# Optimization experiments

Hardware: AMD Instinct MI355X
Metric: run time of the kernel (lower is better)

Reference implementation:

```python
import jax, jax.numpy as jnp
import numpy as np

N, E, D, H = 50000, 500000, 128, 128


def setup_inputs() -> dict:
    key = jax.random.key(0)
    ks = jax.random.split(key, 20)
    s = 0.05
    inp = {
        "node_states": jax.random.normal(ks[0], (N, D), jnp.float32),
        "edge_features": jax.random.normal(ks[1], (E, D), jnp.float32),
        "from_idx": jax.random.randint(ks[2], (E,), 0, N, dtype=jnp.int32),
        "to_idx": jax.random.randint(ks[3], (E,), 0, N, dtype=jnp.int32),
        "graph_idx": jax.random.randint(ks[4], (N,), 0, 16, dtype=jnp.int32),
        # message MLP: Linear(3D,H)-ReLU-Linear(H,H)-ReLU-Linear(H,D)
        "mW1": jax.random.normal(ks[5], (3 * D, H), jnp.float32) * s,
        "mb1": jnp.zeros((H,), jnp.float32),
        "mW2": jax.random.normal(ks[6], (H, H), jnp.float32) * s,
        "mb2": jnp.zeros((H,), jnp.float32),
        "mW3": jax.random.normal(ks[7], (H, D), jnp.float32) * s,
        "mb3": jnp.zeros((D,), jnp.float32),
    }
    # three GRU cells; W: input->gates [D,3D], U: hidden->gates [D,3D]; gate order r,z,n (torch)
    for i, g in enumerate(["g0", "g1", "g2"]):
        inp[g + "W"] = jax.random.normal(ks[8 + 2 * i], (D, 3 * D), jnp.float32) * s
        inp[g + "U"] = jax.random.normal(ks[9 + 2 * i], (D, 3 * D), jnp.float32) * s
        inp[g + "b"] = jnp.zeros((3 * D,), jnp.float32)
        inp[g + "c"] = jnp.zeros((3 * D,), jnp.float32)
    return inp


def _mlp(x, W1, b1, W2, b2, W3, b3):
    h = jax.nn.relu(x @ W1 + b1)
    h = jax.nn.relu(h @ W2 + b2)
    return h @ W3 + b3


def _gru(x, h, W, U, b, c):
    gi = x @ W + b  # [N,3D]
    gh = h @ U + c
    ir, iz, inn = jnp.split(gi, 3, axis=1)
    hr, hz, hn = jnp.split(gh, 3, axis=1)
    r = jax.nn.sigmoid(ir + hr)
    z = jax.nn.sigmoid(iz + hz)
    n = jnp.tanh(inn + r * hn)
    return (1.0 - z) * n + z * h


def reference(node_states, edge_features, from_idx, to_idx, graph_idx,
              mW1, mb1, mW2, mb2, mW3, mb3,
              g0W, g0U, g0b, g0c, g1W, g1U, g1b, g1c, g2W, g2U, g2b, g2c):
    n_nodes = node_states.shape[0]

    def prop_once(fi, ti):
        edge_in = jnp.concatenate(
            [node_states[fi], node_states[ti], edge_features], axis=1)  # [E,3D]
        edge_states = _mlp(edge_in, mW1, mb1, mW2, mb2, mW3, mb3)  # [E,D]
        return jax.ops.segment_sum(edge_states, ti, num_segments=n_nodes)

    # forward uses self.message_net for BOTH directions (reverse net unused)
    agg = prop_once(from_idx, to_idx) + prop_once(to_idx, from_idx)  # [N,D]

    h1 = _gru(node_states, agg, g0W, g0U, g0b, g0c)
    h2 = _gru(agg, h1, g1W, g1U, g1b, g1c)
    h3 = _gru(h1, h2, g2W, g2U, g2b, g2c)
    return h3
```

## Files before the change

kernel.cpp:

```cpp
#include <hip/hip_runtime.h>

typedef unsigned short u16;
typedef __attribute__((ext_vector_type(8))) short bf16x8;
typedef __attribute__((ext_vector_type(4))) float f32x4;

__device__ inline u16 f2bf(float f) {
  unsigned int u = __float_as_uint(f);
  u += 0x7fffu + ((u >> 16) & 1u);
  return (u16)(u >> 16);
}
__device__ inline float bf2f(u16 v) {
  return __uint_as_float((unsigned)v << 16);
}

__device__ inline uint4 pack8(float4 a, float4 b) {
  uint4 r;
  r.x = (unsigned)f2bf(a.x) | ((unsigned)f2bf(a.y) << 16);
  r.y = (unsigned)f2bf(a.z) | ((unsigned)f2bf(a.w) << 16);
  r.z = (unsigned)f2bf(b.x) | ((unsigned)f2bf(b.y) << 16);
  r.w = (unsigned)f2bf(b.z) | ((unsigned)f2bf(b.w) << 16);
  return r;
}

struct TransDesc {
  const float* src[9];
  u16* dst[9];
  int R[9];
  int C[9];
  int pre[10];
};

__global__ void transpose_all_kernel(TransDesc td) {
  int t = blockIdx.x * 256 + threadIdx.x;
  if (t >= td.pre[9]) return;
  int seg = 0;
  while (t >= td.pre[seg + 1]) ++seg;
  int local = t - td.pre[seg];
  int C = td.C[seg], R = td.R[seg];
  int r = local / C, c = local - r * C;
  td.dst[seg][(size_t)c * R + r] = f2bf(td.src[seg][local]);
}

__global__ void count_kernel(const int* __restrict__ fi,
                             const int* __restrict__ ti,
                             int* __restrict__ cnt, int E) {
  int e = blockIdx.x * 256 + threadIdx.x;
  if (e < E) {
    atomicAdd(&cnt[ti[e]], 1);
    atomicAdd(&cnt[fi[e]], 1);
  }
}

__global__ void scan1_kernel(const int* __restrict__ cnt,
                             int* __restrict__ partial, int N, int chunk) {
  __shared__ int sdata[256];
  int b = blockIdx.x, t = threadIdx.x;
  int base = b * chunk;
  int sum = 0;
  for (int i = t; i < chunk; i += 256) {
    int idx = base + i;
    if (idx < N) sum += cnt[idx];
  }
  sdata[t] = sum;
  __syncthreads();
  for (int s2 = 128; s2 > 0; s2 >>= 1) {
    if (t < s2) sdata[t] += sdata[t + s2];
    __syncthreads();
  }
  if (t == 0) partial[b] = sdata[0];
}

__global__ void scan2_kernel(int* __restrict__ partial) {
  __shared__ int s[256];
  int t = threadIdx.x;
  int own = partial[t];
  s[t] = own;
  __syncthreads();
  for (int d2 = 1; d2 < 256; d2 <<= 1) {
    int v = (t >= d2) ? s[t - d2] : 0;
    __syncthreads();
    s[t] += v;
    __syncthreads();
  }
  partial[t] = s[t] - own;
}

__global__ void scan3_kernel(const int* __restrict__ cnt,
                             const int* __restrict__ partialEx,
                             int* __restrict__ cursor, int N, int chunk) {
  __shared__ int s[256];
  int b = blockIdx.x, t = threadIdx.x;
  int base = b * chunk;
  int own = (t < chunk && base + t < N) ? cnt[base + t] : 0;
  s[t] = own;
  __syncthreads();
  for (int d2 = 1; d2 < 256; d2 <<= 1) {
    int v = (t >= d2) ? s[t - d2] : 0;
    __syncthreads();
    s[t] += v;
    __syncthreads();
  }
  int ex = s[t] - own + partialEx[b];
  if (t < chunk && base + t < N) cursor[base + t] = ex;
}

__global__ void slot_kernel(const int* __restrict__ fi,
                            const int* __restrict__ ti,
                            int* __restrict__ cursor, int* __restrict__ s_nbr,
                            int* __restrict__ s_eid, int* __restrict__ s_dest,
                            int E) {
  int e = blockIdx.x * 256 + threadIdx.x;
  if (e < E) {
    int f = fi[e], t2 = ti[e];
    int p0 = atomicAdd(&cursor[t2], 1);
    s_nbr[p0] = f;
    s_eid[p0] = e;
    s_dest[p0] = t2;
    int p1 = atomicAdd(&cursor[f], 1);
    s_nbr[p1] = t2;
    s_eid[p1] = e;
    s_dest[p1] = f;
  }
}

__device__ inline void stage_w_rw(u16* sW, const u16* __restrict__ src,
                                  int roww, int colofs, int tid) {
  int n = tid >> 1, half = tid & 1;
  const u16* s = src + (size_t)n * roww + colofs + half * 64;
#pragma unroll
  for (int q = 0; q < 8; ++q) {
    uint4 v = *(const uint4*)(s + q * 8);
    int byte = n * 256 + ((half * 128 + q * 16) ^ ((n & 7) << 4));
    *(uint4*)((char*)sW + byte) = v;
  }
}

__device__ inline void stage_w_512(u16* sW, const u16* __restrict__ src,
                                   int roww, int colofs, int tid) {
  int n = tid >> 2, quarter = tid & 3;
  const u16* s = src + (size_t)n * roww + colofs + quarter * 32;
#pragma unroll
  for (int q = 0; q < 4; ++q) {
    uint4 v = *(const uint4*)(s + q * 8);
    int byte = n * 256 + ((quarter * 64 + q * 16) ^ ((n & 7) << 4));
    *(uint4*)((char*)sW + byte) = v;
  }
}

__device__ inline void mfma_pass(const u16* A, const u16* W, f32x4 acc[8],
                                 int w, int lane) {
  const int cA = lane & 15;
  const int ko = (lane >> 4) * 8;
  const int arow = 16 * w + cA;
#pragma unroll
  for (int kk = 0; kk < 4; ++kk) {
    int ka = (kk * 32 + ko) * 2;
    int sx = ka ^ ((cA & 7) << 4);
    bf16x8 a = *(const bf16x8*)((const char*)A + arow * 256 + sx);
#pragma unroll
    for (int nt = 0; nt < 8; ++nt) {
      bf16x8 bb = *(const bf16x8*)((const char*)W + (nt * 16 + cA) * 256 + sx);
      acc[nt] = __builtin_amdgcn_mfma_f32_16x16x32_bf16(a, bb, acc[nt], 0, 0, 0);
    }
  }
}

__device__ inline void write_h_lds(u16* sH, const f32x4 acc[8], int w,
                                   int lane) {
#pragma unroll
  for (int nt = 0; nt < 8; ++nt) {
    int col = nt * 16 + (lane & 15);
#pragma unroll
    for (int i = 0; i < 4; ++i) {
      int rr = 16 * w + ((lane >> 4) * 4) + i;
      *(u16*)((char*)sH + rr * 256 + ((col * 2) ^ ((rr & 7) << 4))) =
          f2bf(acc[nt][i]);
    }
  }
}

__global__ __launch_bounds__(256) void gemm1_kernel(
    const float* __restrict__ ns, const float* __restrict__ ef,
    const u16* __restrict__ Wt1, const float* __restrict__ b1,
    u16* __restrict__ Pa, u16* __restrict__ Pb, u16* __restrict__ EFm, int N,
    int E, int Nb) {
  __shared__ u16 sA[64 * 128];
  __shared__ u16 sW[128 * 128];
  const int tid = threadIdx.x;
  const int lane = tid & 63;
  const int w = tid >> 6;
  if ((int)blockIdx.x < Nb) {
    const int r0 = blockIdx.x * 64;
    {
      int row = tid >> 2, seg = tid & 3;
      int rr = r0 + row;
      if (rr >= N) rr = N - 1;
      const float4* sx = (const float4*)(ns + (size_t)rr * 128 + seg * 32);
#pragma unroll
      for (int q = 0; q < 4; ++q) {
        int byte = row * 256 + ((seg * 64 + q * 16) ^ ((row & 7) << 4));
        *(uint4*)((char*)sA + byte) = pack8(sx[q * 2], sx[q * 2 + 1]);
      }
    }
    stage_w_rw(sW, Wt1, 384, 0, tid);
    __syncthreads();
    f32x4 accA[8] = {};
    mfma_pass(sA, sW, accA, w, lane);
    __syncthreads();
    stage_w_rw(sW, Wt1, 384, 128, tid);
    __syncthreads();
    f32x4 accB[8] = {};
    mfma_pass(sA, sW, accB, w, lane);
#pragma unroll
    for (int nt = 0; nt < 8; ++nt) {
      int col = nt * 16 + (lane & 15);
#pragma unroll
      for (int i = 0; i < 4; ++i) {
        int rr = 16 * w + ((lane >> 4) * 4) + i;
        int row = r0 + rr;
        if (row < N) {
          Pa[(size_t)row * 128 + col] = f2bf(accA[nt][i]);
          Pb[(size_t)row * 128 + col] = f2bf(accB[nt][i]);
        }
      }
    }
  } else {
    const int r0 = (blockIdx.x - Nb) * 64;
    {
      int row = tid >> 2, seg = tid & 3;
      int rr = r0 + row;
      if (rr >= E) rr = E - 1;
      const float4* sx = (const float4*)(ef + (size_t)rr * 128 + seg * 32);
#pragma unroll
      for (int q = 0; q < 4; ++q) {
        int byte = row * 256 + ((seg * 64 + q * 16) ^ ((row & 7) << 4));
        *(uint4*)((char*)sA + byte) = pack8(sx[q * 2], sx[q * 2 + 1]);
      }
    }
    stage_w_rw(sW, Wt1, 384, 256, tid);
    __syncthreads();
    f32x4 acc[8] = {};
    mfma_pass(sA, sW, acc, w, lane);
    __syncthreads();
#pragma unroll
    for (int nt = 0; nt < 8; ++nt) {
      int col = nt * 16 + (lane & 15);
      float bv = b1[col];
#pragma unroll
      for (int i = 0; i < 4; ++i) {
        int rr = 16 * w + ((lane >> 4) * 4) + i;
        *(u16*)((char*)sA + rr * 256 + ((col * 2) ^ ((rr & 7) << 4))) =
            f2bf(acc[nt][i] + bv);
      }
    }
    __syncthreads();
#pragma unroll
    for (int it = 0; it < 4; ++it) {
      int task = tid + (it << 8);
      int row = task >> 4, c8 = task & 15;
      int gr = r0 + row;
      if (gr < E) {
        uint4 v = *(const uint4*)((const char*)sA + row * 256 +
                                  ((c8 << 4) ^ ((row & 7) << 4)));
        *(uint4*)(EFm + (size_t)gr * 128 + (c8 << 3)) = v;
      }
    }
  }
}

__global__ __launch_bounds__(512, 2) void edge_csr2_kernel(
    const u16* __restrict__ EFm, const int* __restrict__ s_nbr,
    const int* __restrict__ s_eid, const int* __restrict__ s_dest,
    const u16* __restrict__ Wt2, const u16* __restrict__ Wt3,
    const u16* __restrict__ Pa, const u16* __restrict__ Pb,
    const float* __restrict__ b2, const float* __restrict__ b3,
    float* __restrict__ aggf, int nslots, int ntiles) {
  __shared__ u16 sW2[128 * 128];
  __shared__ u16 sW3[128 * 128];
  __shared__ u16 sH[64 * 128];
  const int tid = threadIdx.x;
  const int lane = tid & 63;
  const int wv = tid >> 6;
  const int mw = wv >> 1;
  const int nw = wv & 1;
  const int l15 = lane & 15;
  const int lhi = lane >> 4;

  stage_w_512(sW2, Wt2, 128, 0, tid);
  stage_w_512(sW3, Wt3, 128, 0, tid);
  float b2f[4], b3f[4];
#pragma unroll
  for (int nt = 0; nt < 4; ++nt) {
    int col = (nw << 6) + (nt << 4) + l15;
    b2f[nt] = b2[col];
    b3f[nt] = b3[col];
  }
  __syncthreads();

  const int ra = (mw << 4) + l15;

  for (int t = blockIdx.x; t < ntiles; t += gridDim.x) {
    const int r0 = t << 6;
#pragma unroll
    for (int it = 0; it < 2; ++it) {
      int task = tid + (it << 9);
      int row = task >> 4;
      int c8 = task & 15;
      int r = r0 + row;
      int rc = r < nslots ? r : nslots - 1;
      int nbr = s_nbr[rc], eid = s_eid[rc], dst = s_dest[rc];
      uint4 efv = *(const uint4*)(EFm + (size_t)eid * 128 + (c8 << 3));
      uint4 pav = *(const uint4*)(Pa + (size_t)nbr * 128 + (c8 << 3));
      uint4 pbv = *(const uint4*)(Pb + (size_t)dst * 128 + (c8 << 3));
      const u16* pe = (const u16*)&efv;
      const u16* pa = (const u16*)&pav;
      const u16* pb = (const u16*)&pbv;
      unsigned o[4];
#pragma unroll
      for (int j = 0; j < 4; ++j) {
        float v0 = fmaxf(bf2f(pe[2 * j]) + bf2f(pa[2 * j]) + bf2f(pb[2 * j]), 0.f);
        float v1 = fmaxf(bf2f(pe[2 * j + 1]) + bf2f(pa[2 * j + 1]) + bf2f(pb[2 * j + 1]), 0.f);
        o[j] = (unsigned)f2bf(v0) | ((unsigned)f2bf(v1) << 16);
      }
      *(uint4*)((char*)sH + row * 256 + ((c8 << 4) ^ ((row & 7) << 4))) = *(uint4*)o;
    }
    __syncthreads();
    bf16x8 hA[4];
#pragma unroll
    for (int kk = 0; kk < 4; ++kk) {
      int sx = ((kk << 6) + (lhi << 4)) ^ ((ra & 7) << 4);
      hA[kk] = *(const bf16x8*)((const char*)sH + ra * 256 + sx);
    }
    f32x4 acc[4] = {};
#pragma unroll
    for (int kk = 0; kk < 4; ++kk) {
#pragma unroll
      for (int nt = 0; nt < 4; ++nt) {
        int c = (nw << 6) + (nt << 4) + l15;
        int sx = ((kk << 6) + (lhi << 4)) ^ ((c & 7) << 4);
        bf16x8 bb = *(const bf16x8*)((const char*)sW2 + c * 256 + sx);
        acc[nt] = __builtin_amdgcn_mfma_f32_16x16x32_bf16(hA[kk], bb, acc[nt], 0, 0, 0);
      }
    }
    __syncthreads();
#pragma unroll
    for (int i = 0; i < 4; ++i) {
      int rl = (mw << 4) + (lhi << 2) + i;
#pragma unroll
      for (int nt = 0; nt < 4; ++nt) {
        int col = (nw << 6) + (nt << 4) + l15;
        float v = fmaxf(acc[nt][i] + b2f[nt], 0.f);
        *(u16*)((char*)sH + rl * 256 + ((col * 2) ^ ((rl & 7) << 4))) = f2bf(v);
        acc[nt][i] = 0.f;
      }
    }
    __syncthreads();
#pragma unroll
    for (int kk = 0; kk < 4; ++kk) {
      int sx = ((kk << 6) + (lhi << 4)) ^ ((ra & 7) << 4);
      hA[kk] = *(const bf16x8*)((const char*)sH + ra * 256 + sx);
    }
#pragma unroll
    for (int kk = 0; kk < 4; ++kk) {
#pragma unroll
      for (int nt = 0; nt < 4; ++nt) {
        int c = (nw << 6) + (nt << 4) + l15;
        int sx = ((kk << 6) + (lhi << 4)) ^ ((c & 7) << 4);
        bf16x8 bb = *(const bf16x8*)((const char*)sW3 + c * 256 + sx);
        acc[nt] = __builtin_amdgcn_mfma_f32_16x16x32_bf16(hA[kk], bb, acc[nt], 0, 0, 0);
      }
    }
    __syncthreads();
#pragma unroll
    for (int i = 0; i < 4; ++i) {
      int rl = (mw << 4) + (lhi << 2) + i;
#pragma unroll
      for (int nt = 0; nt < 4; ++nt) {
        int col = (nw << 6) + (nt << 4) + l15;
        *(u16*)((char*)sH + rl * 256 + ((col * 2) ^ ((rl & 7) << 4))) =
            f2bf(acc[nt][i] + b3f[nt]);
      }
    }
    __syncthreads();
    {
      int c = tid & 127, q = tid >> 7;
      float s = 0.f;
      int prev = -1;
      int rbeg = q << 4;
#pragma unroll 4
      for (int rr = rbeg; rr < rbeg + 16; ++rr) {
        int r = r0 + rr;
        int d = (r < nslots) ? s_dest[r] : -1;
        if (d != prev) {
          if (prev >= 0) unsafeAtomicAdd(&aggf[(size_t)prev * 128 + c], s);
          prev = d;
          s = 0.f;
        }
        if (d >= 0)
          s += bf2f(*(const u16*)((const char*)sH + rr * 256 +
                                  ((c * 2) ^ ((rr & 7) << 4))));
      }
      if (prev >= 0) unsafeAtomicAdd(&aggf[(size_t)prev * 128 + c], s);
    }
    __syncthreads();
  }
}

__global__ __launch_bounds__(512, 1) void gru3_kernel(
    const float* __restrict__ ns, const float* __restrict__ aggf,
    const u16* __restrict__ g0W, const u16* __restrict__ g0U,
    const u16* __restrict__ g1W, const u16* __restrict__ g1U,
    const u16* __restrict__ g2W, const u16* __restrict__ g2U,
    const float* __restrict__ b0, const float* __restrict__ c0,
    const float* __restrict__ b1, const float* __restrict__ c1,
    const float* __restrict__ b2, const float* __restrict__ c2,
    float* __restrict__ out, int N) {
  __shared__ u16 sX[128 * 128];
  __shared__ u16 sG[128 * 128];
  __shared__ u16 sW[128 * 128];
  const int tid = threadIdx.x;
  const int lane = tid & 63;
  const int w = tid >> 6;
  const int r0 = blockIdx.x * 128;
  {
    int row = tid >> 2, seg = tid & 3;
    int rr = r0 + row;
    if (rr >= N) rr = N - 1;
    const float4* sx = (const float4*)(ns + (size_t)rr * 128 + seg * 32);
    const float4* sh = (const float4*)(aggf + (size_t)rr * 128 + seg * 32);
#pragma unroll
    for (int q = 0; q < 4; ++q) {
      int byte = row * 256 + ((seg * 64 + q * 16) ^ ((row & 7) << 4));
      *(uint4*)((char*)sX + byte) = pack8(sx[q * 2], sx[q * 2 + 1]);
      *(uint4*)((char*)sG + byte) = pack8(sh[q * 2], sh[q * 2 + 1]);
    }
  }

  float hpf[8][4];

#define GPASS(SRC, ABUF, ACC)                       \
  __syncthreads();                                  \
  stage_w_512(sW, (SRC), 128, 0, tid);              \
  __syncthreads();                                  \
  mfma_pass((ABUF), sW, (ACC), w, lane);

  {
    f32x4 ar[8] = {}, az[8] = {}, ai[8] = {}, ah[8] = {};
    GPASS(g0W + 0 * 16384, sX, ar)
    GPASS(g0U + 0 * 16384, sG, ar)
    GPASS(g0W + 1 * 16384, sX, az)
    GPASS(g0U + 1 * 16384, sG, az)
    GPASS(g0W + 2 * 16384, sX, ai)
    GPASS(g0U + 2 * 16384, sG, ah)
    f32x4 h1[8];
#pragma unroll
    for (int nt = 0; nt < 8; ++nt) {
      int col = nt * 16 + (lane & 15);
      float brc = b0[col] + c0[col];
      float bzc = b0[128 + col] + c0[128 + col];
      float bi = b0[256 + col];
      float bc2 = c0[256 + col];
#pragma unroll
      for (int i = 0; i < 4; ++i) {
        int rloc = 16 * w + ((lane >> 4) * 4) + i;
        int row = r0 + rloc;
        int rowc = row < N ? row : N - 1;
        float hf = aggf[(size_t)rowc * 128 + col];
        float rg = 1.f / (1.f + __expf(-(ar[nt][i] + brc)));
        float zg = 1.f / (1.f + __expf(-(az[nt][i] + bzc)));
        float pre = ai[nt][i] + bi + rg * (ah[nt][i] + bc2);
        float ng = 2.f / (1.f + __expf(-2.f * pre)) - 1.f;
        float hv = (1.f - zg) * ng + zg * hf;
        h1[nt][i] = hv;
        hpf[nt][i] = hv;
      }
    }
    write_h_lds(sX, h1, w, lane);
  }
  {
    f32x4 ar[8] = {}, az[8] = {}, ai[8] = {}, ah[8] = {};
    GPASS(g1W + 0 * 16384, sG, ar)
    GPASS(g1U + 0 * 16384, sX, ar)
    GPASS(g1W + 1 * 16384, sG, az)
    GPASS(g1U + 1 * 16384, sX, az)
    GPASS(g1W + 2 * 16384, sG, ai)
    GPASS(g1U + 2 * 16384, sX, ah)
    f32x4 h2[8];
#pragma unroll
    for (int nt = 0; nt < 8; ++nt) {
      int col = nt * 16 + (lane & 15);
      float brc = b1[col] + c1[col];
      float bzc = b1[128 + col] + c1[128 + col];
      float bi = b1[256 + col];
      float bc2 = c1[256 + col];
#pragma unroll
      for (int i = 0; i < 4; ++i) {
        float rg = 1.f / (1.f + __expf(-(ar[nt][i] + brc)));
        float zg = 1.f / (1.f + __expf(-(az[nt][i] + bzc)));
        float pre = ai[nt][i] + bi + rg * (ah[nt][i] + bc2);
        float ng = 2.f / (1.f + __expf(-2.f * pre)) - 1.f;
        float hv = (1.f - zg) * ng + zg * hpf[nt][i];
        h2[nt][i] = hv;
        hpf[nt][i] = hv;
      }
    }
    write_h_lds(sG, h2, w, lane);
  }
  {
    f32x4 ar[8] = {}, az[8] = {}, ai[8] = {}, ah[8] = {};
    GPASS(g2W + 0 * 16384, sX, ar)
    GPASS(g2U + 0 * 16384, sG, ar)
    GPASS(g2W + 1 * 16384, sX, az)
    GPASS(g2U + 1 * 16384, sG, az)
    GPASS(g2W + 2 * 16384, sX, ai)
    GPASS(g2U + 2 * 16384, sG, ah)
#pragma unroll
    for (int nt = 0; nt < 8; ++nt) {
      int col = nt * 16 + (lane & 15);
      float brc = b2[col] + c2[col];
      float bzc = b2[128 + col] + c2[128 + col];
      float bi = b2[256 + col];
      float bc2 = c2[256 + col];
#pragma unroll
      for (int i = 0; i < 4; ++i) {
        int rloc = 16 * w + ((lane >> 4) * 4) + i;
        int row = r0 + rloc;
        if (row < N) {
          float rg = 1.f / (1.f + __expf(-(ar[nt][i] + brc)));
          float zg = 1.f / (1.f + __expf(-(az[nt][i] + bzc)));
          float pre = ai[nt][i] + bi + rg * (ah[nt][i] + bc2);
          float ng = 2.f / (1.f + __expf(-2.f * pre)) - 1.f;
          out[(size_t)row * 128 + col] = (1.f - zg) * ng + zg * hpf[nt][i];
        }
      }
    }
  }
#undef GPASS
}

extern "C" void kernel_launch(void* const* d_in, const int* in_sizes, int n_in,
                              void* d_out, int out_size, void* d_ws,
                              size_t ws_size, hipStream_t stream) {
  const float* ns = (const float*)d_in[0];
  const float* ef = (const float*)d_in[1];
  const int* from_idx = (const int*)d_in[2];
  const int* to_idx = (const int*)d_in[3];
  const float* mW1 = (const float*)d_in[5];
  const float* mb1 = (const float*)d_in[6];
  const float* mW2 = (const float*)d_in[7];
  const float* mb2 = (const float*)d_in[8];
  const float* mW3 = (const float*)d_in[9];
  const float* mb3 = (const float*)d_in[10];
  const float* gW[3] = {(const float*)d_in[11], (const float*)d_in[15], (const float*)d_in[19]};
  const float* gU[3] = {(const float*)d_in[12], (const float*)d_in[16], (const float*)d_in[20]};
  const float* gb[3] = {(const float*)d_in[13], (const float*)d_in[17], (const float*)d_in[21]};
  const float* gc[3] = {(const float*)d_in[14], (const float*)d_in[18], (const float*)d_in[22]};

  const int N = in_sizes[0] / 128;
  const int E = in_sizes[1] / 128;
  const int nslots = 2 * E;

  char* base = (char*)d_ws;
  size_t cur = 0;
  auto alloc = [&](size_t bytes) {
    size_t p = cur;
    cur = (cur + bytes + 255) & ~(size_t)255;
    return (void*)(base + p);
  };
  float* aggf = (float*)alloc((size_t)N * 128 * 4);
  u16* Pa = (u16*)alloc((size_t)N * 128 * 2);
  u16* Pb = (u16*)alloc((size_t)N * 128 * 2);
  u16* Wt1 = (u16*)alloc(384 * 128 * 2);
  u16* Wt2 = (u16*)alloc(128 * 128 * 2);
  u16* Wt3 = (u16*)alloc(128 * 128 * 2);
  u16 *gWt[3], *gUt[3];
  for (int i = 0; i < 3; ++i) {
    gWt[i] = (u16*)alloc(384 * 128 * 2);
    gUt[i] = (u16*)alloc(384 * 128 * 2);
  }
  int* cnt = (int*)alloc((size_t)N * 4);
  int* cursor = (int*)alloc((size_t)N * 4);
  int* partial = (int*)alloc(256 * 4);
  int* s_nbr = (int*)alloc((size_t)nslots * 4);
  int* s_eid = (int*)alloc((size_t)nslots * 4);
  int* s_dest = (int*)alloc((size_t)nslots * 4);
  u16* EFm = (u16*)alloc((size_t)E * 128 * 2);
  (void)ws_size;

  {
    TransDesc td;
    const float* srcs[9] = {mW1, mW2, mW3, gW[0], gU[0], gW[1], gU[1], gW[2], gU[2]};
    u16* dsts[9] = {Wt1, Wt2, Wt3, gWt[0], gUt[0], gWt[1], gUt[1], gWt[2], gUt[2]};
    int Rs[9] = {384, 128, 128, 128, 128, 128, 128, 128, 128};
    int Cs[9] = {128, 128, 128, 384, 384, 384, 384, 384, 384};
    int acc = 0;
    for (int i = 0; i < 9; ++i) {
      td.src[i] = srcs[i];
      td.dst[i] = dsts[i];
      td.R[i] = Rs[i];
      td.C[i] = Cs[i];
      td.pre[i] = acc;
      acc += Rs[i] * Cs[i];
    }
    td.pre[9] = acc;
    transpose_all_kernel<<<(acc + 255) / 256, 256, 0, stream>>>(td);
  }

  hipMemsetAsync(cnt, 0, (size_t)N * 4, stream);
  count_kernel<<<(E + 255) / 256, 256, 0, stream>>>(from_idx, to_idx, cnt, E);
  int chunk = (N + 255) / 256;
  scan1_kernel<<<256, 256, 0, stream>>>(cnt, partial, N, chunk);
  scan2_kernel<<<1, 256, 0, stream>>>(partial);
  scan3_kernel<<<256, 256, 0, stream>>>(cnt, partial, cursor, N, chunk);
  slot_kernel<<<(E + 255) / 256, 256, 0, stream>>>(from_idx, to_idx, cursor,
                                                   s_nbr, s_eid, s_dest, E);

  int Nb = (N + 63) / 64, Eb = (E + 63) / 64;
  gemm1_kernel<<<Nb + Eb, 256, 0, stream>>>(ns, ef, Wt1, mb1, Pa, Pb, EFm, N,
                                            E, Nb);

  hipMemsetAsync(aggf, 0, (size_t)N * 128 * 4, stream);
  int ntiles = (nslots + 63) / 64;
  int egrid = ntiles < 512 ? ntiles : 512;
  edge_csr2_kernel<<<egrid, 512, 0, stream>>>(EFm, s_nbr, s_eid, s_dest, Wt2,
                                              Wt3, Pa, Pb, mb2, mb3, aggf,
                                              nslots, ntiles);

  int gblocks = (N + 127) / 128;
  gru3_kernel<<<gblocks, 512, 0, stream>>>(
      ns, aggf, gWt[0], gUt[0], gWt[1], gUt[1], gWt[2], gUt[2], gb[0], gc[0],
      gb[1], gc[1], gb[2], gc[2], (float*)d_out, N);
}
```

Measured before the change: 632.3 us.

## Read GRU weights directly from global and enlarge gemm1 tiles to 128 rows

The GRU kernel no longer stages each weight slice into LDS behind barriers. MFMA B-operands are now read straight from global/L2, with 64-row blocks of 256 threads and two blocks per CU. Gate computation is reordered (r and n first, then z) so fewer accumulator sets are live at once, lowering register pressure. gemm1 now uses 512-thread blocks over 128-row tiles, so each staged weight tile serves twice as many rows. The cost is uncoalesced global weight loads in the GRU, which depend on cache hits.

```diff
diff --git a/kernel.cpp b/kernel.cpp
--- a/kernel.cpp
+++ b/kernel.cpp
@@ -123,18 +123,6 @@
   }
 }
 
-__device__ inline void stage_w_rw(u16* sW, const u16* __restrict__ src,
-                                  int roww, int colofs, int tid) {
-  int n = tid >> 1, half = tid & 1;
-  const u16* s = src + (size_t)n * roww + colofs + half * 64;
-#pragma unroll
-  for (int q = 0; q < 8; ++q) {
-    uint4 v = *(const uint4*)(s + q * 8);
-    int byte = n * 256 + ((half * 128 + q * 16) ^ ((n & 7) << 4));
-    *(uint4*)((char*)sW + byte) = v;
-  }
-}
-
 __device__ inline void stage_w_512(u16* sW, const u16* __restrict__ src,
                                    int roww, int colofs, int tid) {
   int n = tid >> 2, quarter = tid & 3;
@@ -165,6 +153,25 @@
   }
 }
 
+__device__ inline void mfma_pass_g(const u16* A, const u16* __restrict__ Wg,
+                                   f32x4 acc[8], int w, int lane) {
+  const int cA = lane & 15;
+  const int ko = (lane >> 4) * 8;
+  const int arow = 16 * w + cA;
+#pragma unroll
+  for (int kk = 0; kk < 4; ++kk) {
+    int ka = (kk * 32 + ko) * 2;
+    int sx = ka ^ ((cA & 7) << 4);
+    bf16x8 a = *(const bf16x8*)((const char*)A + arow * 256 + sx);
+#pragma unroll
+    for (int nt = 0; nt < 8; ++nt) {
+      bf16x8 bb = *(const bf16x8*)(Wg + (size_t)(nt * 16 + cA) * 128 +
+                                   kk * 32 + ko);
+      acc[nt] = __builtin_amdgcn_mfma_f32_16x16x32_bf16(a, bb, acc[nt], 0, 0, 0);
+    }
+  }
+}
+
 __device__ inline void write_h_lds(u16* sH, const f32x4 acc[8], int w,
                                    int lane) {
 #pragma unroll
@@ -179,18 +186,18 @@
   }
 }
 
-__global__ __launch_bounds__(256) void gemm1_kernel(
+__global__ __launch_bounds__(512) void gemm1_kernel(
     const float* __restrict__ ns, const float* __restrict__ ef,
     const u16* __restrict__ Wt1, const float* __restrict__ b1,
     u16* __restrict__ Pa, u16* __restrict__ Pb, u16* __restrict__ EFm, int N,
     int E, int Nb) {
-  __shared__ u16 sA[64 * 128];
+  __shared__ u16 sA[128 * 128];
   __shared__ u16 sW[128 * 128];
   const int tid = threadIdx.x;
   const int lane = tid & 63;
   const int w = tid >> 6;
   if ((int)blockIdx.x < Nb) {
-    const int r0 = blockIdx.x * 64;
+    const int r0 = blockIdx.x * 128;
     {
       int row = tid >> 2, seg = tid & 3;
       int rr = r0 + row;
@@ -202,12 +209,12 @@
         *(uint4*)((char*)sA + byte) = pack8(sx[q * 2], sx[q * 2 + 1]);
       }
     }
-    stage_w_rw(sW, Wt1, 384, 0, tid);
+    stage_w_512(sW, Wt1, 384, 0, tid);
     __syncthreads();
     f32x4 accA[8] = {};
     mfma_pass(sA, sW, accA, w, lane);
     __syncthreads();
-    stage_w_rw(sW, Wt1, 384, 128, tid);
+    stage_w_512(sW, Wt1, 384, 128, tid);
     __syncthreads();
     f32x4 accB[8] = {};
     mfma_pass(sA, sW, accB, w, lane);
@@ -225,7 +232,7 @@
       }
     }
   } else {
-    const int r0 = (blockIdx.x - Nb) * 64;
+    const int r0 = (blockIdx.x - Nb) * 128;
     {
       int row = tid >> 2, seg = tid & 3;
       int rr = r0 + row;
@@ -237,7 +244,7 @@
         *(uint4*)((char*)sA + byte) = pack8(sx[q * 2], sx[q * 2 + 1]);
       }
     }
-    stage_w_rw(sW, Wt1, 384, 256, tid);
+    stage_w_512(sW, Wt1, 384, 256, tid);
     __syncthreads();
     f32x4 acc[8] = {};
     mfma_pass(sA, sW, acc, w, lane);
@@ -256,7 +263,7 @@
     __syncthreads();
 #pragma unroll
     for (int it = 0; it < 4; ++it) {
-      int task = tid + (it << 8);
+      int task = tid + (it << 9);
       int row = task >> 4, c8 = task & 15;
       int gr = r0 + row;
       if (gr < E) {
@@ -406,7 +413,7 @@
   }
 }
 
-__global__ __launch_bounds__(512, 1) void gru3_kernel(
+__global__ __launch_bounds__(256, 2) void gru3_kernel(
     const float* __restrict__ ns, const float* __restrict__ aggf,
     const u16* __restrict__ g0W, const u16* __restrict__ g0U,
     const u16* __restrict__ g1W, const u16* __restrict__ g1U,
@@ -415,15 +422,17 @@
     const float* __restrict__ b1, const float* __restrict__ c1,
     const float* __restrict__ b2, const float* __restrict__ c2,
     float* __restrict__ out, int N) {
-  __shared__ u16 sX[128 * 128];
-  __shared__ u16 sG[128 * 128];
-  __shared__ u16 sW[128 * 128];
+  __shared__ u16 sX[64 * 128];
+  __shared__ u16 sG[64 * 128];
   const int tid = threadIdx.x;
   const int lane = tid & 63;
   const int w = tid >> 6;
-  const int r0 = blockIdx.x * 128;
+  const int r0 = blockIdx.x * 64;
+  const int l15 = lane & 15;
+
   {
-    int row = tid >> 2, seg = tid & 3;
+    int row = 16 * w + (lane >> 2);
+    int seg = lane & 3;
     int rr = r0 + row;
     if (rr >= N) rr = N - 1;
     const float4* sx = (const float4*)(ns + (size_t)rr * 128 + seg * 32);
@@ -438,104 +447,63 @@
 
   float hpf[8][4];
 
-#define GPASS(SRC, ABUF, ACC)                       \
-  __syncthreads();                                  \
-  stage_w_512(sW, (SRC), 128, 0, tid);              \
-  __syncthreads();                                  \
-  mfma_pass((ABUF), sW, (ACC), w, lane);
+#define GRU_BODY(XL, HL, GW, GU, BB, CC, HP_EXPR, EMIT)                       \
+  {                                                                           \
+    f32x4 gr[8] = {}, gn[8] = {}, hn[8] = {};                                 \
+    mfma_pass_g((XL), (GW) + 0 * 16384, gr, w, lane);                         \
+    mfma_pass_g((HL), (GU) + 0 * 16384, gr, w, lane);                         \
+    mfma_pass_g((XL), (GW) + 2 * 16384, gn, w, lane);                         \
+    mfma_pass_g((HL), (GU) + 2 * 16384, hn, w, lane);                         \
+    _Pragma("unroll") for (int nt = 0; nt < 8; ++nt) {                        \
+      int col = nt * 16 + l15;                                                \
+      float brc = (BB)[col] + (CC)[col];                                      \
+      float bi = (BB)[256 + col];                                             \
+      float bc2 = (CC)[256 + col];                                            \
+      _Pragma("unroll") for (int i = 0; i < 4; ++i) {                         \
+        float rg = 1.f / (1.f + __expf(-(gr[nt][i] + brc)));                  \
+        float pre = gn[nt][i] + bi + rg * (hn[nt][i] + bc2);                  \
+        gn[nt][i] = 2.f / (1.f + __expf(-2.f * pre)) - 1.f;                   \
+      }                                                                       \
+    }                                                                         \
+    _Pragma("unroll") for (int nt = 0; nt < 8; ++nt)                          \
+        _Pragma("unroll") for (int i = 0; i < 4; ++i) gr[nt][i] = 0.f;        \
+    mfma_pass_g((XL), (GW) + 1 * 16384, gr, w, lane);                         \
+    mfma_pass_g((HL), (GU) + 1 * 16384, gr, w, lane);                         \
+    _Pragma("unroll") for (int nt = 0; nt < 8; ++nt) {                        \
+      int col = nt * 16 + l15;                                                \
+      float bzc = (BB)[128 + col] + (CC)[128 + col];                          \
+      _Pragma("unroll") for (int i = 0; i < 4; ++i) {                         \
+        float zg = 1.f / (1.f + __expf(-(gr[nt][i] + bzc)));                  \
+        float hv = (1.f - zg) * gn[nt][i] + zg * (HP_EXPR);                   \
+        EMIT;                                                                 \
+      }                                                                       \
+    }                                                                         \
+  }
 
   {
-    f32x4 ar[8] = {}, az[8] = {}, ai[8] = {}, ah[8] = {};
-    GPASS(g0W + 0 * 16384, sX, ar)
-    GPASS(g0U + 0 * 16384, sG, ar)
-    GPASS(g0W + 1 * 16384, sX, az)
-    GPASS(g0U + 1 * 16384, sG, az)
-    GPASS(g0W + 2 * 16384, sX, ai)
-    GPASS(g0U + 2 * 16384, sG, ah)
     f32x4 h1[8];
-#pragma unroll
-    for (int nt = 0; nt < 8; ++nt) {
-      int col = nt * 16 + (lane & 15);
-      float brc = b0[col] + c0[col];
-      float bzc = b0[128 + col] + c0[128 + col];
-      float bi = b0[256 + col];
-      float bc2 = c0[256 + col];
-#pragma unroll
-      for (int i = 0; i < 4; ++i) {
-        int rloc = 16 * w + ((lane >> 4) * 4) + i;
-        int row = r0 + rloc;
-        int rowc = row < N ? row : N - 1;
-        float hf = aggf[(size_t)rowc * 128 + col];
-        float rg = 1.f / (1.f + __expf(-(ar[nt][i] + brc)));
-        float zg = 1.f / (1.f + __expf(-(az[nt][i] + bzc)));
-        float pre = ai[nt][i] + bi + rg * (ah[nt][i] + bc2);
-        float ng = 2.f / (1.f + __expf(-2.f * pre)) - 1.f;
-        float hv = (1.f - zg) * ng + zg * hf;
-        h1[nt][i] = hv;
-        hpf[nt][i] = hv;
-      }
-    }
+    GRU_BODY(sX, sG, g0W, g0U, b0, c0,
+             aggf[(size_t)(r0 + 16 * w + ((lane >> 4) << 2) + i < N
+                               ? r0 + 16 * w + ((lane >> 4) << 2) + i
+                               : N - 1) * 128 + col],
+             { h1[nt][i] = hv; hpf[nt][i] = hv; })
     write_h_lds(sX, h1, w, lane);
   }
   {
-    f32x4 ar[8] = {}, az[8] = {}, ai[8] = {}, ah[8] = {};
-    GPASS(g1W + 0 * 16384, sG, ar)
-    GPASS(g1U + 0 * 16384, sX, ar)
-    GPASS(g1W + 1 * 16384, sG, az)
-    GPASS(g1U + 1 * 16384, sX, az)
-    GPASS(g1W + 2 * 16384, sG, ai)
-    GPASS(g1U + 2 * 16384, sX, ah)
     f32x4 h2[8];
-#pragma unroll
-    for (int nt = 0; nt < 8; ++nt) {
-      int col = nt * 16 + (lane & 15);
-      float brc = b1[col] + c1[col];
-      float bzc = b1[128 + col] + c1[128 + col];
-      float bi = b1[256 + col];
-      float bc2 = c1[256 + col];
-#pragma unroll
-      for (int i = 0; i < 4; ++i) {
-        float rg = 1.f / (1.f + __expf(-(ar[nt][i] + brc)));
-        float zg = 1.f / (1.f + __expf(-(az[nt][i] + bzc)));
-        float pre = ai[nt][i] + bi + rg * (ah[nt][i] + bc2);
-        float ng = 2.f / (1.f + __expf(-2.f * pre)) - 1.f;
-        float hv = (1.f - zg) * ng + zg * hpf[nt][i];
-        h2[nt][i] = hv;
-        hpf[nt][i] = hv;
-      }
-    }
+    GRU_BODY(sG, sX, g1W, g1U, b1, c1, hpf[nt][i],
+             { h2[nt][i] = hv; })
     write_h_lds(sG, h2, w, lane);
-  }
-  {
-    f32x4 ar[8] = {}, az[8] = {}, ai[8] = {}, ah[8] = {};
-    GPASS(g2W + 0 * 16384, sX, ar)
-    GPASS(g2U + 0 * 16384, sG, ar)
-    GPASS(g2W + 1 * 16384, sX, az)
-    GPASS(g2U + 1 * 16384, sG, az)
-    GPASS(g2W + 2 * 16384, sX, ai)
-    GPASS(g2U + 2 * 16384, sG, ah)
-#pragma unroll
-    for (int nt = 0; nt < 8; ++nt) {
-      int col = nt * 16 + (lane & 15);
-      float brc = b2[col] + c2[col];
-      float bzc = b2[128 + col] + c2[128 + col];
-      float bi = b2[256 + col];
-      float bc2 = c2[256 + col];
-#pragma unroll
-      for (int i = 0; i < 4; ++i) {
-        int rloc = 16 * w + ((lane >> 4) * 4) + i;
-        int row = r0 + rloc;
-        if (row < N) {
-          float rg = 1.f / (1.f + __expf(-(ar[nt][i] + brc)));
-          float zg = 1.f / (1.f + __expf(-(az[nt][i] + bzc)));
-          float pre = ai[nt][i] + bi + rg * (ah[nt][i] + bc2);
-          float ng = 2.f / (1.f + __expf(-2.f * pre)) - 1.f;
-          out[(size_t)row * 128 + col] = (1.f - zg) * ng + zg * hpf[nt][i];
-        }
-      }
-    }
-  }
-#undef GPASS
+#pragma unroll
+    for (int nt = 0; nt < 8; ++nt)
+#pragma unroll
+      for (int i = 0; i < 4; ++i) hpf[nt][i] = h2[nt][i];
+  }
+  GRU_BODY(sX, sG, g2W, g2U, b2, c2, hpf[nt][i], {
+    int row = r0 + 16 * w + ((lane >> 4) << 2) + i;
+    if (row < N) out[(size_t)row * 128 + col] = hv;
+  })
+#undef GRU_BODY
 }
 
 extern "C" void kernel_launch(void* const* d_in, const int* in_sizes, int n_in,
@@ -615,8 +583,8 @@
   slot_kernel<<<(E + 255) / 256, 256, 0, stream>>>(from_idx, to_idx, cursor,
                                                    s_nbr, s_eid, s_dest, E);
 
-  int Nb = (N + 63) / 64, Eb = (E + 63) / 64;
-  gemm1_kernel<<<Nb + Eb, 256, 0, stream>>>(ns, ef, Wt1, mb1, Pa, Pb, EFm, N,
+  int Nb = (N + 127) / 128, Eb = (E + 127) / 128;
+  gemm1_kernel<<<Nb + Eb, 512, 0, stream>>>(ns, ef, Wt1, mb1, Pa, Pb, EFm, N,
                                             E, Nb);
 
   hipMemsetAsync(aggf, 0, (size_t)N * 128 * 4, stream);
@@ -626,8 +594,8 @@
                                               Wt3, Pa, Pb, mb2, mb3, aggf,
                                               nslots, ntiles);
 
-  int gblocks = (N + 127) / 128;
-  gru3_kernel<<<gblocks, 512, 0, stream>>>(
+  int gblocks = (N + 63) / 64;
+  gru3_kernel<<<gblocks, 256, 0, stream>>>(
       ns, aggf, gWt[0], gUt[0], gWt[1], gUt[1], gWt[2], gUt[2], gb[0], gc[0],
       gb[1], gc[1], gb[2], gc[2], (float*)d_out, N);
 }
```

Measured after the change: 825.8 us. 30.6% more time.

## Double-buffer GRU weight staging and enlarge gemm1 tiles to 128 rows

Applied to the files above, without the earlier changes.

The GRU kernel now double-buffers weight tiles in LDS, loading the next weight slab while MFMA runs on the current one. This removes one barrier per pass and the exposed staging latency. The first-layer GEMM kernel now processes 128-row tiles with 512 threads, halving the number of weight restages per row. The cost is more LDS per block, which may reduce occupancy.

```diff
diff --git a/kernel.cpp b/kernel.cpp
--- a/kernel.cpp
+++ b/kernel.cpp
@@ -123,18 +123,6 @@
   }
 }
 
-__device__ inline void stage_w_rw(u16* sW, const u16* __restrict__ src,
-                                  int roww, int colofs, int tid) {
-  int n = tid >> 1, half = tid & 1;
-  const u16* s = src + (size_t)n * roww + colofs + half * 64;
-#pragma unroll
-  for (int q = 0; q < 8; ++q) {
-    uint4 v = *(const uint4*)(s + q * 8);
-    int byte = n * 256 + ((half * 128 + q * 16) ^ ((n & 7) << 4));
-    *(uint4*)((char*)sW + byte) = v;
-  }
-}
-
 __device__ inline void stage_w_512(u16* sW, const u16* __restrict__ src,
                                    int roww, int colofs, int tid) {
   int n = tid >> 2, quarter = tid & 3;
@@ -179,18 +167,18 @@
   }
 }
 
-__global__ __launch_bounds__(256) void gemm1_kernel(
+__global__ __launch_bounds__(512) void gemm1_kernel(
     const float* __restrict__ ns, const float* __restrict__ ef,
     const u16* __restrict__ Wt1, const float* __restrict__ b1,
     u16* __restrict__ Pa, u16* __restrict__ Pb, u16* __restrict__ EFm, int N,
     int E, int Nb) {
-  __shared__ u16 sA[64 * 128];
+  __shared__ u16 sA[128 * 128];
   __shared__ u16 sW[128 * 128];
   const int tid = threadIdx.x;
   const int lane = tid & 63;
   const int w = tid >> 6;
   if ((int)blockIdx.x < Nb) {
-    const int r0 = blockIdx.x * 64;
+    const int r0 = blockIdx.x * 128;
     {
       int row = tid >> 2, seg = tid & 3;
       int rr = r0 + row;
@@ -202,12 +190,12 @@
         *(uint4*)((char*)sA + byte) = pack8(sx[q * 2], sx[q * 2 + 1]);
       }
     }
-    stage_w_rw(sW, Wt1, 384, 0, tid);
+    stage_w_512(sW, Wt1, 384, 0, tid);
     __syncthreads();
     f32x4 accA[8] = {};
     mfma_pass(sA, sW, accA, w, lane);
     __syncthreads();
-    stage_w_rw(sW, Wt1, 384, 128, tid);
+    stage_w_512(sW, Wt1, 384, 128, tid);
     __syncthreads();
     f32x4 accB[8] = {};
     mfma_pass(sA, sW, accB, w, lane);
@@ -225,7 +213,7 @@
       }
     }
   } else {
-    const int r0 = (blockIdx.x - Nb) * 64;
+    const int r0 = (blockIdx.x - Nb) * 128;
     {
       int row = tid >> 2, seg = tid & 3;
       int rr = r0 + row;
@@ -237,7 +225,7 @@
         *(uint4*)((char*)sA + byte) = pack8(sx[q * 2], sx[q * 2 + 1]);
       }
     }
-    stage_w_rw(sW, Wt1, 384, 256, tid);
+    stage_w_512(sW, Wt1, 384, 256, tid);
     __syncthreads();
     f32x4 acc[8] = {};
     mfma_pass(sA, sW, acc, w, lane);
@@ -256,7 +244,7 @@
     __syncthreads();
 #pragma unroll
     for (int it = 0; it < 4; ++it) {
-      int task = tid + (it << 8);
+      int task = tid + (it << 9);
       int row = task >> 4, c8 = task & 15;
       int gr = r0 + row;
       if (gr < E) {
@@ -417,7 +405,7 @@
     float* __restrict__ out, int N) {
   __shared__ u16 sX[128 * 128];
   __shared__ u16 sG[128 * 128];
-  __shared__ u16 sW[128 * 128];
+  __shared__ u16 sW[2][128 * 128];
   const int tid = threadIdx.x;
   const int lane = tid & 63;
   const int w = tid >> 6;
@@ -436,22 +424,31 @@
     }
   }
 
+  const u16* wseq[18] = {
+      g0W,          g0U,          g0W + 16384, g0U + 16384, g0W + 32768, g0U + 32768,
+      g1W,          g1U,          g1W + 16384, g1U + 16384, g1W + 32768, g1U + 32768,
+      g2W,          g2U,          g2W + 16384, g2U + 16384, g2W + 32768, g2U + 32768};
+
+  stage_w_512(sW[0], wseq[0], 128, 0, tid);
+  __syncthreads();
+
   float hpf[8][4];
 
-#define GPASS(SRC, ABUF, ACC)                       \
-  __syncthreads();                                  \
-  stage_w_512(sW, (SRC), 128, 0, tid);              \
-  __syncthreads();                                  \
-  mfma_pass((ABUF), sW, (ACC), w, lane);
+#define PIPE_PASS(PH, ABUF, ACC)                                    \
+  {                                                                 \
+    if ((PH) + 1 < 18) stage_w_512(sW[((PH) + 1) & 1], wseq[(PH) + 1], 128, 0, tid); \
+    mfma_pass((ABUF), sW[(PH) & 1], (ACC), w, lane);                \
+    __syncthreads();                                                \
+  }
 
   {
     f32x4 ar[8] = {}, az[8] = {}, ai[8] = {}, ah[8] = {};
-    GPASS(g0W + 0 * 16384, sX, ar)
-    GPASS(g0U + 0 * 16384, sG, ar)
-    GPASS(g0W + 1 * 16384, sX, az)
-    GPASS(g0U + 1 * 16384, sG, az)
-    GPASS(g0W + 2 * 16384, sX, ai)
-    GPASS(g0U + 2 * 16384, sG, ah)
+    PIPE_PASS(0, sX, ar)
+    PIPE_PASS(1, sG, ar)
+    PIPE_PASS(2, sX, az)
+    PIPE_PASS(3, sG, az)
+    PIPE_PASS(4, sX, ai)
+    PIPE_PASS(5, sG, ah)
     f32x4 h1[8];
 #pragma unroll
     for (int nt = 0; nt < 8; ++nt) {
@@ -479,12 +476,12 @@
   }
   {
     f32x4 ar[8] = {}, az[8] = {}, ai[8] = {}, ah[8] = {};
-    GPASS(g1W + 0 * 16384, sG, ar)
-    GPASS(g1U + 0 * 16384, sX, ar)
-    GPASS(g1W + 1 * 16384, sG, az)
-    GPASS(g1U + 1 * 16384, sX, az)
-    GPASS(g1W + 2 * 16384, sG, ai)
-    GPASS(g1U + 2 * 16384, sX, ah)
+    PIPE_PASS(6, sG, ar)
+    PIPE_PASS(7, sX, ar)
+    PIPE_PASS(8, sG, az)
+    PIPE_PASS(9, sX, az)
+    PIPE_PASS(10, sG, ai)
+    PIPE_PASS(11, sX, ah)
     f32x4 h2[8];
 #pragma unroll
     for (int nt = 0; nt < 8; ++nt) {
@@ -508,12 +505,12 @@
   }
   {
     f32x4 ar[8] = {}, az[8] = {}, ai[8] = {}, ah[8] = {};
-    GPASS(g2W + 0 * 16384, sX, ar)
-    GPASS(g2U + 0 * 16384, sG, ar)
-    GPASS(g2W + 1 * 16384, sX, az)
-    GPASS(g2U + 1 * 16384, sG, az)
-    GPASS(g2W + 2 * 16384, sX, ai)
-    GPASS(g2U + 2 * 16384, sG, ah)
+    PIPE_PASS(12, sX, ar)
+    PIPE_PASS(13, sG, ar)
+    PIPE_PASS(14, sX, az)
+    PIPE_PASS(15, sG, az)
+    PIPE_PASS(16, sX, ai)
+    PIPE_PASS(17, sG, ah)
 #pragma unroll
     for (int nt = 0; nt < 8; ++nt) {
       int col = nt * 16 + (lane & 15);
@@ -535,7 +532,7 @@
       }
     }
   }
-#undef GPASS
+#undef PIPE_PASS
 }
 
 extern "C" void kernel_launch(void* const* d_in, const int* in_sizes, int n_in,
@@ -615,8 +612,8 @@
   slot_kernel<<<(E + 255) / 256, 256, 0, stream>>>(from_idx, to_idx, cursor,
                                                    s_nbr, s_eid, s_dest, E);
 
-  int Nb = (N + 63) / 64, Eb = (E + 63) / 64;
-  gemm1_kernel<<<Nb + Eb, 256, 0, stream>>>(ns, ef, Wt1, mb1, Pa, Pb, EFm, N,
+  int Nb = (N + 127) / 128, Eb = (E + 127) / 128;
+  gemm1_kernel<<<Nb + Eb, 512, 0, stream>>>(ns, ef, Wt1, mb1, Pa, Pb, EFm, N,
                                             E, Nb);
 
   hipMemsetAsync(aggf, 0, (size_t)N * 128 * 4, stream);
```

After: 598.1 us (median of 2 runs). -5.4%, faster.
